# Kernel tuning notes

Measured on AMD Instinct MI355X. Metric: run time of the kernel, lower is better.

## Reference

```python
import jax, jax.numpy as jnp
import numpy as np


def _fake_quant(x, scale, qmin, qmax):
    # per-tensor int8 fake quant: scale -> round -> clamp -> dequant
    q = jnp.clip(jnp.round(x / scale), qmin, qmax)
    return q * scale


def setup_inputs() -> dict:
    key = jax.random.key(0)
    k1, k2, k3 = jax.random.split(key, 3)
    B, IN, OUT = 4096, 2048, 8192
    x = jax.random.normal(k1, (B, IN), dtype=jnp.float32)
    weight = jax.random.normal(k2, (OUT, IN), dtype=jnp.float32) * 0.02
    bias = jax.random.normal(k3, (OUT,), dtype=jnp.float32) * 0.01
    mul_val = jnp.full((1,), 200.0, dtype=jnp.float32)
    return {"x": x, "weight": weight, "bias": bias, "mul_val": mul_val}


def reference(x, weight, bias, mul_val):
    # Int8ActPerTensorFloat: signed, non-narrow range [-128, 127]
    act_scale = jnp.max(jnp.abs(x)) / 128.0
    xq = _fake_quant(x, act_scale, -128.0, 127.0)
    # Int8WeightPerTensorFloat: signed, narrow range [-127, 127]
    w_scale = jnp.max(jnp.abs(weight)) / 127.0
    wq = _fake_quant(weight, w_scale, -127.0, 127.0)
    # linear: y = xq @ wq.T + b, then elementwise scalar multiply
    y = jnp.einsum("bi,oi->bo", xq, wq) + bias
    return mul_val * y
```

## Files before the change

kernel.cpp:

```cpp
#include <hip/hip_runtime.h>


typedef int v4i  __attribute__((ext_vector_type(4)));
typedef int v16i __attribute__((ext_vector_type(16)));

#define MDIM 4096
#define NDIM 8192
#define KDIM 2048
#define NT   (KDIM / 64)

typedef __attribute__((address_space(1))) void* gas_ptr;
typedef __attribute__((address_space(3))) void* las_ptr;

#define XBLK 1024

__global__ __launch_bounds__(256) void absmax2(const float4* __restrict__ x,
                                               const float4* __restrict__ w,
                                               float* __restrict__ partial) {
    const int tid = threadIdx.x;
    const bool isx = blockIdx.x < XBLK;
    float m0 = 0.0f, m1 = 0.0f;
    if (isx) {
        const size_t base = (size_t)blockIdx.x * 256 + tid;
#pragma unroll
        for (int j = 0; j < 8; j += 2) {
            float4 v0 = x[base + (size_t)j * 262144];
            float4 v1 = x[base + (size_t)(j + 1) * 262144];
            m0 = fmaxf(m0, fmaxf(fmaxf(fabsf(v0.x), fabsf(v0.y)),
                                 fmaxf(fabsf(v0.z), fabsf(v0.w))));
            m1 = fmaxf(m1, fmaxf(fmaxf(fabsf(v1.x), fabsf(v1.y)),
                                 fmaxf(fabsf(v1.z), fabsf(v1.w))));
        }
    } else {
        const size_t base = (size_t)(blockIdx.x - XBLK) * 256 + tid;
#pragma unroll
        for (int j = 0; j < 8; j += 2) {
            float4 v0 = w[base + (size_t)j * 524288];
            float4 v1 = w[base + (size_t)(j + 1) * 524288];
            m0 = fmaxf(m0, fmaxf(fmaxf(fabsf(v0.x), fabsf(v0.y)),
                                 fmaxf(fabsf(v0.z), fabsf(v0.w))));
            m1 = fmaxf(m1, fmaxf(fmaxf(fabsf(v1.x), fabsf(v1.y)),
                                 fmaxf(fabsf(v1.z), fabsf(v1.w))));
        }
    }
    float m = fmaxf(m0, m1);
#pragma unroll
    for (int off = 32; off > 0; off >>= 1)
        m = fmaxf(m, __shfl_xor(m, off, 64));
    __shared__ float wm[4];
    if ((tid & 63) == 0) wm[tid >> 6] = m;
    __syncthreads();
    if (tid == 0)
        partial[blockIdx.x] = fmaxf(fmaxf(wm[0], wm[1]), fmaxf(wm[2], wm[3]));
}

__global__ __launch_bounds__(256) void quant2(const float4* __restrict__ x,
                                              v4i* __restrict__ qxp,
                                              const float4* __restrict__ w,
                                              v4i* __restrict__ qwp,
                                              const float* __restrict__ partial,
                                              unsigned* __restrict__ scales) {
    const int tid = threadIdx.x;
    float gx = 0.0f, gw = 0.0f;
#pragma unroll
    for (int j = 0; j < 4; ++j) gx = fmaxf(gx, partial[tid + j * 256]);
#pragma unroll
    for (int j = 0; j < 8; ++j) gw = fmaxf(gw, partial[XBLK + tid + j * 256]);
#pragma unroll
    for (int off = 32; off > 0; off >>= 1) {
        gx = fmaxf(gx, __shfl_xor(gx, off, 64));
        gw = fmaxf(gw, __shfl_xor(gw, off, 64));
    }
    __shared__ float smx[4], smw[4];
    if ((tid & 63) == 0) { smx[tid >> 6] = gx; smw[tid >> 6] = gw; }
    __syncthreads();
    const float fmx = fmaxf(fmaxf(smx[0], smx[1]), fmaxf(smx[2], smx[3]));
    const float fmw = fmaxf(fmaxf(smw[0], smw[1]), fmaxf(smw[2], smw[3]));
    if (blockIdx.x == 0 && tid == 0) {
        scales[0] = __float_as_uint(fmx);
        scales[1] = __float_as_uint(fmw);
    }
    const float sxs = fmx / 128.0f;
    const float sws = fmw / 127.0f;

    const bool isx = blockIdx.x < XBLK;
    const float4* in = isx ? x : w;
    v4i* outp = isx ? qxp : qwp;
    const int total = isx ? (MDIM * KDIM / 16) : (NDIM * KDIM / 16);
    const int nb = isx ? XBLK : (3072 - XBLK);
    const int b  = isx ? blockIdx.x : (blockIdx.x - XBLK);
    const float s  = isx ? sxs : sws;
    const float lo = isx ? -128.0f : -127.0f;
    for (int idx = b * 256 + tid; idx < total; idx += nb * 256) {
        const int c   = idx & 3;
        const int r   = (idx >> 2) & 255;
        const int kt  = (idx >> 10) & 31;
        const int blk = idx >> 15;
        const float4* src = in + (size_t)(blk * 256 + r) * (KDIM / 4) + kt * 16 + c * 4;
        int q[4];
#pragma unroll
        for (int j = 0; j < 4; ++j) {
            float4 v = src[j];
            int b0 = (int)fminf(fmaxf(rintf(v.x / s), lo), 127.0f);
            int b1 = (int)fminf(fmaxf(rintf(v.y / s), lo), 127.0f);
            int b2 = (int)fminf(fmaxf(rintf(v.z / s), lo), 127.0f);
            int b3 = (int)fminf(fmaxf(rintf(v.w / s), lo), 127.0f);
            q[j] = (b0 & 255) | ((b1 & 255) << 8) | ((b2 & 255) << 16) | (b3 << 24);
        }
        v4i qq; qq[0] = q[0]; qq[1] = q[1]; qq[2] = q[2]; qq[3] = q[3];
        outp[((size_t)(blk * 32 + kt) * 4 + c) * 256 + r] = qq;
    }
}

__global__ __launch_bounds__(512, 2) void gemm_i8(
    const signed char* __restrict__ qxp, const signed char* __restrict__ qwp,
    const float* __restrict__ bias, const float* __restrict__ mulv,
    const unsigned* __restrict__ scales, float* __restrict__ out) {
    __shared__ signed char ldsA[4][16384];
    __shared__ signed char ldsB[4][16384];

    const int t    = threadIdx.x;
    const int lane = t & 63;
    const int ln   = lane & 31;
    const int hi   = lane >> 5;
    const int w    = t >> 6;
    const int wr   = w >> 2;
    const int wc   = w & 3;

    const int orig = blockIdx.x;
    const int xcd  = orig & 7;
    const int idx  = orig >> 3;
    const int bm   = (xcd & 1) * 8 + (idx >> 3);
    const int bn   = (xcd >> 1) * 8 + (idx & 7);

    const signed char* srcA = qxp + (size_t)bm * (32 * 16384);
    const signed char* srcB = qwp + (size_t)bn * (32 * 16384);
    signed char* dA = &ldsA[0][0] + t * 16;
    signed char* dB = &ldsB[0][0] + t * 16;

    auto stage = [&](int kt) {
        if (kt >= NT) return;
        const int buf = kt & 3;
        const signed char* sa = srcA + kt * 16384 + t * 16;
        const signed char* sb = srcB + kt * 16384 + t * 16;
        __builtin_amdgcn_global_load_lds((gas_ptr)sa,          (las_ptr)(dA + buf * 16384),        16, 0, 0);
        __builtin_amdgcn_global_load_lds((gas_ptr)(sa + 8192), (las_ptr)(dA + buf * 16384 + 8192), 16, 0, 0);
        __builtin_amdgcn_global_load_lds((gas_ptr)sb,          (las_ptr)(dB + buf * 16384),        16, 0, 0);
        __builtin_amdgcn_global_load_lds((gas_ptr)(sb + 8192), (las_ptr)(dB + buf * 16384 + 8192), 16, 0, 0);
    };

    const int aOff = (wr * 128 + ln) * 16;
    const int bOff = (wc * 64  + ln) * 16;

#define READ12(A0, B0, A1, B1, KT) do {                                       \
        const signed char* _Ab = &ldsA[(KT) & 3][0];                          \
        const signed char* _Bb = &ldsB[(KT) & 3][0];                          \
        const signed char* _A0 = _Ab + hi * 4096 + aOff;                      \
        const signed char* _B0 = _Bb + hi * 4096 + bOff;                      \
        const signed char* _A1 = _Ab + (2 + hi) * 4096 + aOff;                \
        const signed char* _B1 = _Bb + (2 + hi) * 4096 + bOff;                \
        A0[0] = *(const v4i*)(_A0);        A0[1] = *(const v4i*)(_A0 + 512);  \
        A0[2] = *(const v4i*)(_A0 + 1024); A0[3] = *(const v4i*)(_A0 + 1536); \
        B0[0] = *(const v4i*)(_B0);        B0[1] = *(const v4i*)(_B0 + 512);  \
        A1[0] = *(const v4i*)(_A1);        A1[1] = *(const v4i*)(_A1 + 512);  \
        A1[2] = *(const v4i*)(_A1 + 1024); A1[3] = *(const v4i*)(_A1 + 1536); \
        B1[0] = *(const v4i*)(_B1);        B1[1] = *(const v4i*)(_B1 + 512);  \
    } while (0)

#define MFMA16(A0, B0, A1, B1) do {                                           \
        __builtin_amdgcn_s_setprio(1);                                        \
        acc[0][0] = __builtin_amdgcn_mfma_i32_32x32x32_i8(A0[0], B0[0], acc[0][0], 0, 0, 0); \
        acc[0][1] = __builtin_amdgcn_mfma_i32_32x32x32_i8(A0[0], B0[1], acc[0][1], 0, 0, 0); \
        acc[1][0] = __builtin_amdgcn_mfma_i32_32x32x32_i8(A0[1], B0[0], acc[1][0], 0, 0, 0); \
        acc[1][1] = __builtin_amdgcn_mfma_i32_32x32x32_i8(A0[1], B0[1], acc[1][1], 0, 0, 0); \
        acc[2][0] = __builtin_amdgcn_mfma_i32_32x32x32_i8(A0[2], B0[0], acc[2][0], 0, 0, 0); \
        acc[2][1] = __builtin_amdgcn_mfma_i32_32x32x32_i8(A0[2], B0[1], acc[2][1], 0, 0, 0); \
        acc[3][0] = __builtin_amdgcn_mfma_i32_32x32x32_i8(A0[3], B0[0], acc[3][0], 0, 0, 0); \
        acc[3][1] = __builtin_amdgcn_mfma_i32_32x32x32_i8(A0[3], B0[1], acc[3][1], 0, 0, 0); \
        acc[0][0] = __builtin_amdgcn_mfma_i32_32x32x32_i8(A1[0], B1[0], acc[0][0], 0, 0, 0); \
        acc[0][1] = __builtin_amdgcn_mfma_i32_32x32x32_i8(A1[0], B1[1], acc[0][1], 0, 0, 0); \
        acc[1][0] = __builtin_amdgcn_mfma_i32_32x32x32_i8(A1[1], B1[0], acc[1][0], 0, 0, 0); \
        acc[1][1] = __builtin_amdgcn_mfma_i32_32x32x32_i8(A1[1], B1[1], acc[1][1], 0, 0, 0); \
        acc[2][0] = __builtin_amdgcn_mfma_i32_32x32x32_i8(A1[2], B1[0], acc[2][0], 0, 0, 0); \
        acc[2][1] = __builtin_amdgcn_mfma_i32_32x32x32_i8(A1[2], B1[1], acc[2][1], 0, 0, 0); \
        acc[3][0] = __builtin_amdgcn_mfma_i32_32x32x32_i8(A1[3], B1[0], acc[3][0], 0, 0, 0); \
        acc[3][1] = __builtin_amdgcn_mfma_i32_32x32x32_i8(A1[3], B1[1], acc[3][1], 0, 0, 0); \
        __builtin_amdgcn_s_setprio(0);                                        \
    } while (0)

    v16i acc[4][2];
#pragma unroll
    for (int mt = 0; mt < 4; ++mt)
#pragma unroll
        for (int nt = 0; nt < 2; ++nt)
#pragma unroll
            for (int r = 0; r < 16; ++r) acc[mt][nt][r] = 0;

    v4i f0A0[4], f0B0[2], f0A1[4], f0B1[2];
    v4i f1A0[4], f1B0[2], f1A1[4], f1B1[2];

    stage(0); stage(1); stage(2);
    asm volatile("s_waitcnt vmcnt(4)" ::: "memory");
    __builtin_amdgcn_s_barrier();
    READ12(f0A0, f0B0, f0A1, f0B1, 0);

    for (int j = 0; j < 15; ++j) {
        const int kt0 = 2 * j;
        stage(kt0 + 3);
        READ12(f1A0, f1B0, f1A1, f1B1, kt0 + 1);
        MFMA16(f0A0, f0B0, f0A1, f0B1);
        asm volatile("s_waitcnt vmcnt(4)" ::: "memory");
        __builtin_amdgcn_s_barrier();
        stage(kt0 + 4);
        READ12(f0A0, f0B0, f0A1, f0B1, kt0 + 2);
        MFMA16(f1A0, f1B0, f1A1, f1B1);
        if (j < 14) asm volatile("s_waitcnt vmcnt(4)" ::: "memory");
        else        asm volatile("s_waitcnt vmcnt(0)" ::: "memory");
        __builtin_amdgcn_s_barrier();
    }
    READ12(f1A0, f1B0, f1A1, f1B1, 31);
    MFMA16(f0A0, f0B0, f0A1, f0B1);
    MFMA16(f1A0, f1B0, f1A1, f1B1);

    const float fm = mulv[0];
    const float fs = fm * (__uint_as_float(scales[0]) / 128.0f)
                        * (__uint_as_float(scales[1]) / 127.0f);
    const int colb = bn * 256 + wc * 64 + ln;
    const int hi4  = hi * 4;
#pragma unroll
    for (int nt = 0; nt < 2; ++nt) {
        const int ocol = colb + nt * 32;
        const float bv = bias[ocol] * fm;
#pragma unroll
        for (int mt = 0; mt < 4; ++mt) {
            float* op = out + (size_t)(bm * 256 + wr * 128 + mt * 32) * NDIM + ocol;
#pragma unroll
            for (int r = 0; r < 16; ++r) {
                const int row = (r & 3) + 8 * (r >> 2) + hi4;
                __builtin_nontemporal_store(fs * (float)acc[mt][nt][r] + bv,
                                            op + (size_t)row * NDIM);
            }
        }
    }
#undef READ12
#undef MFMA16
}

extern "C" void kernel_launch(void* const* d_in, const int* in_sizes, int n_in,
                              void* d_out, int out_size, void* d_ws, size_t ws_size,
                              hipStream_t stream) {
    const float4* x    = (const float4*)d_in[0];
    const float4* wgt  = (const float4*)d_in[1];
    const float*  bias = (const float*)d_in[2];
    const float*  mulv = (const float*)d_in[3];
    float* out = (float*)d_out;

    unsigned* scales  = (unsigned*)d_ws;
    float*    partial = (float*)((char*)d_ws + 256);
    signed char* qxp  = (signed char*)d_ws + 256 + 16384;
    signed char* qwp  = qxp + (size_t)MDIM * KDIM;

    absmax2<<<3072, 256, 0, stream>>>(x, wgt, partial);
    quant2<<<3072, 256, 0, stream>>>(x, (v4i*)qxp, wgt, (v4i*)qwp,
                                     partial, scales);
    gemm_i8<<<512, 512, 0, stream>>>(qxp, qwp, bias, mulv, scales, out);
}
```

Baseline: 123.2 us.

## Load B operand directly from global into registers, dropping B LDS staging

The weight (B) tile is no longer staged through LDS. Each wave now prefetches its B fragments straight from global memory into registers one k-step ahead, while A stays on the 4-deep LDS ring. This halves LDS usage and LDS traffic, which could allow better occupancy and fewer LDS reads. In exchange, each wave issues redundant global loads for B, since waves sharing the same columns each read it, and the vmcnt accounting and pipelining become more fragile, with the B load latency now exposed to the MFMA loop.

New measurement: 127.4 us. 1.03x slower.

```diff
diff --git a/kernel.cpp b/kernel.cpp
--- a/kernel.cpp
+++ b/kernel.cpp
@@ -117,7 +117,6 @@
     const float* __restrict__ bias, const float* __restrict__ mulv,
     const unsigned* __restrict__ scales, float* __restrict__ out) {
     __shared__ signed char ldsA[4][16384];
-    __shared__ signed char ldsB[4][16384];
 
     const int t    = threadIdx.x;
     const int lane = t & 63;
@@ -136,58 +135,66 @@
     const signed char* srcA = qxp + (size_t)bm * (32 * 16384);
     const signed char* srcB = qwp + (size_t)bn * (32 * 16384);
     signed char* dA = &ldsA[0][0] + t * 16;
-    signed char* dB = &ldsB[0][0] + t * 16;
 
     auto stage = [&](int kt) {
         if (kt >= NT) return;
         const int buf = kt & 3;
         const signed char* sa = srcA + kt * 16384 + t * 16;
-        const signed char* sb = srcB + kt * 16384 + t * 16;
         __builtin_amdgcn_global_load_lds((gas_ptr)sa,          (las_ptr)(dA + buf * 16384),        16, 0, 0);
         __builtin_amdgcn_global_load_lds((gas_ptr)(sa + 8192), (las_ptr)(dA + buf * 16384 + 8192), 16, 0, 0);
-        __builtin_amdgcn_global_load_lds((gas_ptr)sb,          (las_ptr)(dB + buf * 16384),        16, 0, 0);
-        __builtin_amdgcn_global_load_lds((gas_ptr)(sb + 8192), (las_ptr)(dB + buf * 16384 + 8192), 16, 0, 0);
     };
 
     const int aOff = (wr * 128 + ln) * 16;
-    const int bOff = (wc * 64  + ln) * 16;
-
-#define READ12(A0, B0, A1, B1, KT) do {                                       \
-        const signed char* _Ab = &ldsA[(KT) & 3][0];                          \
-        const signed char* _Bb = &ldsB[(KT) & 3][0];                          \
-        const signed char* _A0 = _Ab + hi * 4096 + aOff;                      \
-        const signed char* _B0 = _Bb + hi * 4096 + bOff;                      \
-        const signed char* _A1 = _Ab + (2 + hi) * 4096 + aOff;                \
-        const signed char* _B1 = _Bb + (2 + hi) * 4096 + bOff;                \
+    const signed char* gB = srcB + hi * 4096 + (wc * 64 + ln) * 16;
+
+#define READA(A0, A1, KT) do {                                                \
+        const signed char* _A = &ldsA[(KT) & 3][0] + aOff;                    \
+        const signed char* _A0 = _A + hi * 4096;                              \
+        const signed char* _A1 = _A + (2 + hi) * 4096;                        \
         A0[0] = *(const v4i*)(_A0);        A0[1] = *(const v4i*)(_A0 + 512);  \
         A0[2] = *(const v4i*)(_A0 + 1024); A0[3] = *(const v4i*)(_A0 + 1536); \
-        B0[0] = *(const v4i*)(_B0);        B0[1] = *(const v4i*)(_B0 + 512);  \
         A1[0] = *(const v4i*)(_A1);        A1[1] = *(const v4i*)(_A1 + 512);  \
         A1[2] = *(const v4i*)(_A1 + 1024); A1[3] = *(const v4i*)(_A1 + 1536); \
-        B1[0] = *(const v4i*)(_B1);        B1[1] = *(const v4i*)(_B1 + 512);  \
-    } while (0)
-
-#define MFMA16(A0, B0, A1, B1) do {                                           \
+    } while (0)
+
+#define BPF(BR, KT) do {                                                      \
+        const signed char* _B = gB + (size_t)(KT) * 16384;                    \
+        BR[0] = *(const v4i*)(_B);                               \
+        BR[1] = *(const v4i*)(_B + 512);                         \
+        BR[2] = *(const v4i*)(_B + 8192);                        \
+        BR[3] = *(const v4i*)(_B + 8704);                        \
+    } while (0)
+
+#define MFMA16(A0, A1, B) do {                                                \
         __builtin_amdgcn_s_setprio(1);                                        \
-        acc[0][0] = __builtin_amdgcn_mfma_i32_32x32x32_i8(A0[0], B0[0], acc[0][0], 0, 0, 0); \
-        acc[0][1] = __builtin_amdgcn_mfma_i32_32x32x32_i8(A0[0], B0[1], acc[0][1], 0, 0, 0); \
-        acc[1][0] = __builtin_amdgcn_mfma_i32_32x32x32_i8(A0[1], B0[0], acc[1][0], 0, 0, 0); \
-        acc[1][1] = __builtin_amdgcn_mfma_i32_32x32x32_i8(A0[1], B0[1], acc[1][1], 0, 0, 0); \
-        acc[2][0] = __builtin_amdgcn_mfma_i32_32x32x32_i8(A0[2], B0[0], acc[2][0], 0, 0, 0); \
-        acc[2][1] = __builtin_amdgcn_mfma_i32_32x32x32_i8(A0[2], B0[1], acc[2][1], 0, 0, 0); \
-        acc[3][0] = __builtin_amdgcn_mfma_i32_32x32x32_i8(A0[3], B0[0], acc[3][0], 0, 0, 0); \
-        acc[3][1] = __builtin_amdgcn_mfma_i32_32x32x32_i8(A0[3], B0[1], acc[3][1], 0, 0, 0); \
-        acc[0][0] = __builtin_amdgcn_mfma_i32_32x32x32_i8(A1[0], B1[0], acc[0][0], 0, 0, 0); \
-        acc[0][1] = __builtin_amdgcn_mfma_i32_32x32x32_i8(A1[0], B1[1], acc[0][1], 0, 0, 0); \
-        acc[1][0] = __builtin_amdgcn_mfma_i32_32x32x32_i8(A1[1], B1[0], acc[1][0], 0, 0, 0); \
-        acc[1][1] = __builtin_amdgcn_mfma_i32_32x32x32_i8(A1[1], B1[1], acc[1][1], 0, 0, 0); \
-        acc[2][0] = __builtin_amdgcn_mfma_i32_32x32x32_i8(A1[2], B1[0], acc[2][0], 0, 0, 0); \
-        acc[2][1] = __builtin_amdgcn_mfma_i32_32x32x32_i8(A1[2], B1[1], acc[2][1], 0, 0, 0); \
-        acc[3][0] = __builtin_amdgcn_mfma_i32_32x32x32_i8(A1[3], B1[0], acc[3][0], 0, 0, 0); \
-        acc[3][1] = __builtin_amdgcn_mfma_i32_32x32x32_i8(A1[3], B1[1], acc[3][1], 0, 0, 0); \
+        acc[0][0] = __builtin_amdgcn_mfma_i32_32x32x32_i8(A0[0], B[0], acc[0][0], 0, 0, 0); \
+        acc[0][1] = __builtin_amdgcn_mfma_i32_32x32x32_i8(A0[0], B[1], acc[0][1], 0, 0, 0); \
+        acc[1][0] = __builtin_amdgcn_mfma_i32_32x32x32_i8(A0[1], B[0], acc[1][0], 0, 0, 0); \
+        acc[1][1] = __builtin_amdgcn_mfma_i32_32x32x32_i8(A0[1], B[1], acc[1][1], 0, 0, 0); \
+        acc[2][0] = __builtin_amdgcn_mfma_i32_32x32x32_i8(A0[2], B[0], acc[2][0], 0, 0, 0); \
+        acc[2][1] = __builtin_amdgcn_mfma_i32_32x32x32_i8(A0[2], B[1], acc[2][1], 0, 0, 0); \
+        acc[3][0] = __builtin_amdgcn_mfma_i32_32x32x32_i8(A0[3], B[0], acc[3][0], 0, 0, 0); \
+        acc[3][1] = __builtin_amdgcn_mfma_i32_32x32x32_i8(A0[3], B[1], acc[3][1], 0, 0, 0); \
+        acc[0][0] = __builtin_amdgcn_mfma_i32_32x32x32_i8(A1[0], B[2], acc[0][0], 0, 0, 0); \
+        acc[0][1] = __builtin_amdgcn_mfma_i32_32x32x32_i8(A1[0], B[3], acc[0][1], 0, 0, 0); \
+        acc[1][0] = __builtin_amdgcn_mfma_i32_32x32x32_i8(A1[1], B[2], acc[1][0], 0, 0, 0); \
+        acc[1][1] = __builtin_amdgcn_mfma_i32_32x32x32_i8(A1[1], B[3], acc[1][1], 0, 0, 0); \
+        acc[2][0] = __builtin_amdgcn_mfma_i32_32x32x32_i8(A1[2], B[2], acc[2][0], 0, 0, 0); \
+        acc[2][1] = __builtin_amdgcn_mfma_i32_32x32x32_i8(A1[2], B[3], acc[2][1], 0, 0, 0); \
+        acc[3][0] = __builtin_amdgcn_mfma_i32_32x32x32_i8(A1[3], B[2], acc[3][0], 0, 0, 0); \
+        acc[3][1] = __builtin_amdgcn_mfma_i32_32x32x32_i8(A1[3], B[3], acc[3][1], 0, 0, 0); \
         __builtin_amdgcn_s_setprio(0);                                        \
     } while (0)
 
+#define PHASE(KT, STK, PFK, BUSE, BPREF) do {                                 \
+        v4i _a0[4], _a1[4];                                                   \
+        READA(_a0, _a1, KT);                                                  \
+        stage(STK);                                                           \
+        if ((PFK) < NT) BPF(BPREF, PFK);                                      \
+        __builtin_amdgcn_s_barrier();                                         \
+        MFMA16(_a0, _a1, BUSE);                                               \
+    } while (0)
+
     v16i acc[4][2];
 #pragma unroll
     for (int mt = 0; mt < 4; ++mt)
@@ -196,31 +203,25 @@
 #pragma unroll
             for (int r = 0; r < 16; ++r) acc[mt][nt][r] = 0;
 
-    v4i f0A0[4], f0B0[2], f0A1[4], f0B1[2];
-    v4i f1A0[4], f1B0[2], f1A1[4], f1B1[2];
-
+    v4i B0r[4], B1r[4];
+
+    BPF(B0r, 0);
     stage(0); stage(1); stage(2);
-    asm volatile("s_waitcnt vmcnt(4)" ::: "memory");
+    asm volatile("s_waitcnt vmcnt(2)" ::: "memory");
     __builtin_amdgcn_s_barrier();
-    READ12(f0A0, f0B0, f0A1, f0B1, 0);
 
     for (int j = 0; j < 15; ++j) {
         const int kt0 = 2 * j;
-        stage(kt0 + 3);
-        READ12(f1A0, f1B0, f1A1, f1B1, kt0 + 1);
-        MFMA16(f0A0, f0B0, f0A1, f0B1);
-        asm volatile("s_waitcnt vmcnt(4)" ::: "memory");
+        PHASE(kt0,     kt0 + 3, kt0 + 1, B0r, B1r);
         __builtin_amdgcn_s_barrier();
-        stage(kt0 + 4);
-        READ12(f0A0, f0B0, f0A1, f0B1, kt0 + 2);
-        MFMA16(f1A0, f1B0, f1A1, f1B1);
-        if (j < 14) asm volatile("s_waitcnt vmcnt(4)" ::: "memory");
-        else        asm volatile("s_waitcnt vmcnt(0)" ::: "memory");
+        PHASE(kt0 + 1, kt0 + 4, kt0 + 2, B1r, B0r);
+        if (j < 14) asm volatile("s_waitcnt vmcnt(6)" ::: "memory");
+        else        asm volatile("s_waitcnt vmcnt(4)" ::: "memory");
         __builtin_amdgcn_s_barrier();
     }
-    READ12(f1A0, f1B0, f1A1, f1B1, 31);
-    MFMA16(f0A0, f0B0, f0A1, f0B1);
-    MFMA16(f1A0, f1B0, f1A1, f1B1);
+    PHASE(30, NT, 31, B0r, B1r);
+    __builtin_amdgcn_s_barrier();
+    PHASE(31, NT, NT, B1r, B0r);
 
     const float fm = mulv[0];
     const float fs = fm * (__uint_as_float(scales[0]) / 128.0f)
@@ -242,8 +243,10 @@
             }
         }
     }
-#undef READ12
+#undef READA
+#undef BPF
 #undef MFMA16
+#undef PHASE
 }
 
 extern "C" void kernel_launch(void* const* d_in, const int* in_sizes, int n_in,
```
